# Kernel tuning notes

Measured on AMD Instinct MI355X. Metric: run time of the kernel, lower is better.

## Reference

```python
import jax, jax.numpy as jnp
import numpy as np

WIN = (4, 16)
HEADS = 4
DIM = 128
HID = 512

def _rel_index(win):
    ch = np.arange(win[0]); cw = np.arange(win[1])
    coords = np.stack(np.meshgrid(ch, cw, indexing='ij')).reshape(2, -1)  # 2, N
    rel = (coords[:, :, None] - coords[:, None, :]).transpose(1, 2, 0).astype(np.int64)  # N,N,2
    rel[:, :, 0] += win[0] - 1
    rel[:, :, 1] += win[1] - 1
    rel[:, :, 0] *= 2 * win[1] - 1
    return jnp.asarray(rel.sum(-1))  # (N, N) int

REL_IDX = _rel_index(WIN)

def _ln(x, g, b):
    m = x.mean(-1, keepdims=True)
    v = ((x - m) ** 2).mean(-1, keepdims=True)
    return (x - m) / jnp.sqrt(v + 1e-5) * g + b

def _gelu(x):
    return jax.nn.gelu(x, approximate=False)

def _posconv3d(x, w, b):
    # depthwise 3x3x3 conv with singleton depth axis; x: B,C,H,W; w: C,1,3,3,3
    y = jax.lax.conv_general_dilated(x[:, :, None], w, (1, 1, 1), ((1, 1), (1, 1), (1, 1)),
                                     feature_group_count=x.shape[1],
                                     dimension_numbers=('NCDHW', 'OIDHW', 'NCDHW'))
    return y[:, :, 0] + b[None, :, None, None]

def _dwconv2d(x, w, b):
    # depthwise 3x3 conv; x: B,Ch,H,W; w: Ch,1,3,3
    y = jax.lax.conv_general_dilated(x, w, (1, 1), ((1, 1), (1, 1)),
                                     feature_group_count=x.shape[1],
                                     dimension_numbers=('NCHW', 'OIHW', 'NCHW'))
    return y + b[None, :, None, None]

def setup_inputs() -> dict:
    key = jax.random.key(0)
    ks = jax.random.split(key, 12)
    B, C, H, W = 4, DIM, 192, 192
    s = 0.02
    return {
        'x': jax.random.normal(ks[0], (B, C, H, W), jnp.float32),
        'pos_w': jax.random.normal(ks[1], (C, 1, 3, 3, 3), jnp.float32) * s,
        'pos_b': jnp.zeros((C,), jnp.float32),
        'ln1_g': jnp.ones((C,), jnp.float32),
        'ln1_b': jnp.zeros((C,), jnp.float32),
        'q_w': jax.random.normal(ks[2], (C, C), jnp.float32) * s,
        'q_b': jnp.zeros((C,), jnp.float32),
        'kv_w': jax.random.normal(ks[3], (C, 2 * C), jnp.float32) * s,
        'kv_b': jnp.zeros((2 * C,), jnp.float32),
        'rpb': jax.random.normal(ks[4], ((2 * WIN[0] - 1) * (2 * WIN[1] - 1), HEADS), jnp.float32) * s,
        'proj_w': jax.random.normal(ks[5], (C, C), jnp.float32) * s,
        'proj_b': jnp.zeros((C,), jnp.float32),
        'fft1_w': jax.random.normal(ks[6], (2 * C, 2 * C), jnp.float32) * s,
        'fft1_b': jnp.zeros((2 * C,), jnp.float32),
        'fft2_w': jax.random.normal(ks[7], (2 * C, 2 * C), jnp.float32) * s,
        'fft2_b': jnp.zeros((2 * C,), jnp.float32),
        'ln2_g': jnp.ones((C,), jnp.float32),
        'ln2_b': jnp.zeros((C,), jnp.float32),
        'l1_w': jax.random.normal(ks[8], (C, HID), jnp.float32) * s,
        'l1_b': jnp.zeros((HID,), jnp.float32),
        'dw_w': jax.random.normal(ks[9], (HID, 1, 3, 3), jnp.float32) * s,
        'dw_b': jnp.zeros((HID,), jnp.float32),
        'l2_w': jax.random.normal(ks[10], (HID, C), jnp.float32) * s,
        'l2_b': jnp.zeros((C,), jnp.float32),
    }

def _forward(x, pos_w, pos_b, ln1_g, ln1_b, q_w, q_b, kv_w, kv_b, rpb, proj_w, proj_b,
             fft1_w, fft1_b, fft2_w, fft2_b, ln2_g, ln2_b, l1_w, l1_b, dw_w, dw_b, l2_w, l2_b):
    B, C, H, W = x.shape
    wh, ww = WIN
    N = wh * ww
    hd = C // HEADS
    # depthwise 3D positional embedding
    x = x + _posconv3d(x, pos_w, pos_b)
    xt = x.transpose(0, 2, 3, 1)  # B,H,W,C
    shortcut = xt
    xn = _ln(xt, ln1_g, ln1_b)
    # window partition: (B*nW, N, C)  (idx=0 -> no shift, no mask)
    win = xn.reshape(B, H // wh, wh, W // ww, ww, C).transpose(0, 1, 3, 2, 4, 5).reshape(-1, N, C)
    q = (win @ q_w + q_b).reshape(-1, N, HEADS, hd).transpose(0, 2, 1, 3)  # Bw,h,N,d
    kv = (win @ kv_w + kv_b).reshape(-1, N, 2, HEADS, hd).transpose(2, 0, 3, 1, 4)
    k, v = kv[0], kv[1]
    attn = jnp.einsum('bhnd,bhmd->bhnm', q * (hd ** -0.5), k)
    rel_bias = rpb[REL_IDX].transpose(2, 0, 1)  # heads,N,N
    attn = jax.nn.softmax(attn + rel_bias[None], axis=-1)
    out = jnp.einsum('bhnm,bhmd->bhnd', attn, v).transpose(0, 2, 1, 3).reshape(-1, N, C)
    out = out @ proj_w + proj_b
    out = out.reshape(B, H // wh, W // ww, wh, ww, C).transpose(0, 1, 3, 2, 4, 5).reshape(B, H, W, C)
    xt = shortcut + out
    # FFT residual branch (two 1x1 convs on cat(real,imag))
    xc = xt.transpose(0, 3, 1, 2)  # B,C,H,W
    f = jnp.fft.rfft2(xc, axes=(-2, -1))
    ff = jnp.concatenate([f.real, f.imag], axis=1)  # B,2C,H,Wf
    ff = jnp.einsum('bchw,co->bohw', ff, fft1_w) + fft1_b[None, :, None, None]
    ff = jnp.where(ff >= 0, ff, 0.01 * ff)  # LeakyReLU(0.01)
    ff = jnp.einsum('bchw,co->bohw', ff, fft2_w) + fft2_b[None, :, None, None]
    fr, fi = jnp.split(ff, 2, axis=1)
    y = jnp.fft.irfft2(fr + 1j * fi, s=(H, W), axes=(-2, -1))
    xt = xt + y.transpose(0, 2, 3, 1)
    # LeFF: linear -> dwconv -> linear, on full (H,W) grid
    xn2 = _ln(xt, ln2_g, ln2_b)
    h1 = _gelu(xn2 @ l1_w + l1_b)               # B,H,W,HID
    h1 = _gelu(_dwconv2d(h1.transpose(0, 3, 1, 2), dw_w, dw_b))
    h2 = h1.transpose(0, 2, 3, 1) @ l2_w + l2_b  # B,H,W,C
    xt = xt + h2
    return xt.transpose(0, 3, 1, 2)

def reference(x, pos_w, pos_b, ln1_g, ln1_b, q_w, q_b, kv_w, kv_b, rpb, proj_w, proj_b,
              fft1_w, fft1_b, fft2_w, fft2_b, ln2_g, ln2_b, l1_w, l1_b, dw_w, dw_b, l2_w, l2_b):
    return _forward(x, pos_w, pos_b, ln1_g, ln1_b, q_w, q_b, kv_w, kv_b, rpb, proj_w, proj_b,
                    fft1_w, fft1_b, fft2_w, fft2_b, ln2_g, ln2_b, l1_w, l1_b, dw_w, dw_b, l2_w, l2_b)
```

## Files before the change

kernel.cpp:

```cpp
#include <hip/hip_runtime.h>
#include <hip/hip_bf16.h>
#include <math.h>

#define C_DIM 128
#define HGT 192
#define WID 192
#define NB 4
#define WFD 97

#define T_BIAS  0
#define T_QKVB  16384
#define TF_SZ   16896
#define UT_MW    0
#define UT_MHF   49152
#define UT_MHI   196608
#define UT_MWI   344064
#define UT_QKVW  387072
#define UT_PROJW 436224
#define UT_FFT1W 452608
#define UT_FFT2W 518144
#define UT_L1W   583680
#define UT_L2W   649216
#define UT_TOT   714752
#define TAB_SZ   374272

typedef __attribute__((ext_vector_type(8))) short bf16x8;
typedef __attribute__((ext_vector_type(4))) float f32x4;

__device__ __forceinline__ float gelu_f(float v){
  return 0.5f*v*(1.0f + erff(v*0.70710678118654752440f));
}
__device__ __forceinline__ unsigned short f2bf(float f){
  __hip_bfloat16 h = __float2bfloat16(f);
  return *reinterpret_cast<unsigned short*>(&h);
}
__device__ __forceinline__ float bf2f(unsigned short u){
  unsigned int x = ((unsigned int)u)<<16;
  return __uint_as_float(x);
}
__device__ __forceinline__ void st8u(unsigned short* d, bf16x8 v){
  unsigned int* wp = (unsigned int*)&v;
  unsigned int* dp = (unsigned int*)d;
  dp[0]=wp[0]; dp[1]=wp[1]; dp[2]=wp[2]; dp[3]=wp[3];
}

__global__ __launch_bounds__(256) void build_tables(float* __restrict__ tab,
        const float* __restrict__ rpb, const float* __restrict__ q_b, const float* __restrict__ kv_b,
        const float* __restrict__ q_w, const float* __restrict__ kv_w, const float* __restrict__ proj_w,
        const float* __restrict__ fft1_w, const float* __restrict__ fft2_w,
        const float* __restrict__ l1_w, const float* __restrict__ l2_w){
  int idx = blockIdx.x*256 + threadIdx.x;
  const float STEP = (float)(6.283185307179586476925286766559/192.0);
  if (idx < 16384){
    int head = idx>>12, n = (idx>>6)&63, m = idx&63;
    int dh = n/16 - m/16 + 3;
    int dw = (n&15) - (m&15) + 15;
    tab[T_BIAS+idx] = rpb[(dh*31+dw)*4 + head];
    return;
  }
  idx -= 16384;
  if (idx < 384){
    tab[T_QKVB+idx] = (idx < 128) ? q_b[idx] : kv_b[idx-128];
    return;
  }
  idx -= 384;
  unsigned short* ut = (unsigned short*)(tab + TF_SZ);
  if (idx < 49152){
    int r = idx/192, w = idx%192;
    float v = 0.f;
    if (r < 97){ int a = (r*w)%192; v = cosf(a*STEP); }
    else if (r < 194){ int a = ((r-97)*w)%192; v = -sinf(a*STEP); }
    ut[UT_MW+idx] = f2bf(v);
    return;
  }
  idx -= 49152;
  if (idx < 147456){
    int r = idx/384, j = idx%384;
    int hf = (r < 192) ? r : r-192;
    int h  = (j < 192) ? j : j-192;
    int a = (hf*h)%192;
    float c = cosf(a*STEP), s = sinf(a*STEP);
    float v;
    if (r < 192) v = (j < 192) ? c : s;
    else         v = (j < 192) ? -s : c;
    ut[UT_MHF+idx] = f2bf(v);
    return;
  }
  idx -= 147456;
  if (idx < 147456){
    int r = idx/384, j = idx%384;
    int h  = (r < 192) ? r : r-192;
    int hf = (j < 192) ? j : j-192;
    int a = (h*hf)%192;
    float c = cosf(a*STEP), s = sinf(a*STEP);
    float v;
    if (r < 192) v = (j < 192) ? c : -s;
    else         v = (j < 192) ? s : c;
    ut[UT_MHI+idx] = f2bf(v);
    return;
  }
  idx -= 147456;
  if (idx < 43008){
    int w = idx/224, j = idx%224;
    float v = 0.f;
    if (j < 97){
      int a = (j*w)%192;
      float sc = ((j==0 || j==96) ? 1.f : 2.f) / 36864.f;
      v = sc*cosf(a*STEP);
    } else if (j >= 112 && j < 209){
      int k = j-112;
      int a = (k*w)%192;
      float sc = ((k==0 || k==96) ? 1.f : 2.f) / 36864.f;
      v = -sc*sinf(a*STEP);
    }
    ut[UT_MWI+idx] = f2bf(v);
    return;
  }
  idx -= 43008;
  if (idx < 49152){
    int n = idx/128, k = idx%128;
    float v = (n < 128) ? q_w[(size_t)k*128 + n] : kv_w[(size_t)k*256 + (n-128)];
    ut[UT_QKVW+idx] = f2bf(v);
    return;
  }
  idx -= 49152;
  if (idx < 16384){
    int n = idx/128, k = idx%128;
    ut[UT_PROJW+idx] = f2bf(proj_w[(size_t)k*128 + n]);
    return;
  }
  idx -= 16384;
  if (idx < 65536){
    int n = idx/256, k = idx%256;
    ut[UT_FFT1W+idx] = f2bf(fft1_w[(size_t)k*256 + n]);
    return;
  }
  idx -= 65536;
  if (idx < 65536){
    int n = idx/256, k = idx%256;
    ut[UT_FFT2W+idx] = f2bf(fft2_w[(size_t)k*256 + n]);
    return;
  }
  idx -= 65536;
  if (idx < 65536){
    int n = idx/128, k = idx%128;
    ut[UT_L1W+idx] = f2bf(l1_w[(size_t)k*512 + n]);
    return;
  }
  idx -= 65536;
  if (idx < 65536){
    int n = idx/512, k = idx%512;
    ut[UT_L2W+idx] = f2bf(l2_w[(size_t)k*128 + n]);
  }
}

__global__ __launch_bounds__(256) void posconv3_kernel(const float* __restrict__ x, const float* __restrict__ pw,
                               const float* __restrict__ pb, float* __restrict__ xt){
  __shared__ float rows_s[16*340];
  int w0 = blockIdx.x*32, h0 = blockIdx.y*8;
  int b = blockIdx.z >> 3, cb = (blockIdx.z & 7)*16;
  int tid = threadIdx.x;
  int hl = tid >> 5, wl = tid & 31;
  for (int e = tid; e < 16*340; e += 256){
    int c = e / 340; int rem = e - c*340;
    int r = rem / 34; int wc = rem - r*34;
    int gh = h0 - 1 + r, gw = w0 - 1 + wc;
    float v = 0.f;
    if (gh >= 0 && gh < HGT && gw >= 0 && gw < WID)
      v = x[((size_t)(b*C_DIM + cb + c))*(HGT*WID) + gh*WID + gw];
    rows_s[e] = v;
  }
  __syncthreads();
  float outr[16];
  #pragma unroll
  for (int c = 0; c < 16; ++c){
    const float* rs = &rows_s[c*340];
    float wreg[9];
    #pragma unroll
    for (int t9 = 0; t9 < 9; ++t9) wreg[t9] = pw[(cb+c)*27 + 9 + t9];
    float bias = pb[cb+c];
    float acc = rs[(hl+1)*34 + wl+1] + bias;
    #pragma unroll
    for (int ky = 0; ky < 3; ++ky)
      #pragma unroll
      for (int kx = 0; kx < 3; ++kx)
        acc += wreg[ky*3+kx]*rs[(hl+ky)*34 + wl+kx];
    outr[c] = acc;
  }
  __syncthreads();
  {
    int px = hl*32 + wl;
    #pragma unroll
    for (int c = 0; c < 16; ++c) rows_s[px*17 + c] = outr[c];
  }
  __syncthreads();
  for (int r = 0; r < 16; ++r){
    int e = r*256 + tid;
    int cl = e & 15, hw = e >> 4;
    int h = hw >> 5, w = hw & 31;
    xt[((size_t)(b*HGT + h0+h)*WID + (w0+w))*C_DIM + cb + cl] = rows_s[hw*17 + cl];
  }
}

__global__ __launch_bounds__(256) void ln_stats_kernel(const float* __restrict__ src, float* __restrict__ stats){
  int wave = threadIdx.x >> 6; int lane = threadIdx.x & 63;
  size_t p = (size_t)blockIdx.x*4 + wave;
  const float* s = src + p*C_DIM;
  float v0 = s[lane], v1 = s[lane+64];
  float sum = v0 + v1;
  #pragma unroll
  for (int o=1; o<64; o<<=1) sum += __shfl_xor(sum, o, 64);
  float m = sum * (1.0f/128.0f);
  float d0 = v0-m, d1 = v1-m;
  float vs = d0*d0 + d1*d1;
  #pragma unroll
  for (int o=1; o<64; o<<=1) vs += __shfl_xor(vs, o, 64);
  float rstd = rsqrtf(vs*(1.0f/128.0f) + 1e-5f);
  if (lane==0){ stats[2*p] = m; stats[2*p+1] = rstd; }
}

template<int ACT, bool ADD, bool LNA, bool ABF, bool OBF, int NT>
__global__ __launch_bounds__(256) void gemm2(const void* __restrict__ A1v,
                            const unsigned short* __restrict__ WT, const float* __restrict__ bias,
                            void* __restrict__ dstv, int K, int N, int lda,
                            const float* __restrict__ stats, const float* __restrict__ lng,
                            const float* __restrict__ lnb, int prow0, int pmax){
  __shared__ __align__(16) unsigned short As[64*40];
  __shared__ __align__(16) unsigned short Bs[NT][64*40];
  int p0 = blockIdx.y*64, n00 = blockIdx.x*(64*NT);
  int tid = threadIdx.x;
  int wave = tid >> 6, lane = tid & 63;
  int wr = (wave>>1)*32, wc = (wave&1)*32;
  f32x4 acc[NT][4];
  #pragma unroll
  for (int nt=0; nt<NT; ++nt)
    #pragma unroll
    for (int q=0; q<4; ++q) acc[nt][q] = (f32x4){};
  int am = tid >> 2, ak = (tid & 3)*8;
  int brow = tid >> 2, bkk = (tid & 3)*8;
  for (int k0 = 0; k0 < K; k0 += 32){
    if constexpr (ABF){
      const unsigned short* A1u = (const unsigned short*)A1v;
      bf16x8 av = *(const bf16x8*)(A1u + (size_t)(p0+am)*lda + k0 + ak);
      st8u(&As[am*40 + ak], av);
    } else {
      int gp = p0 + am;
      float s0 = 0.f, s1 = 0.f;
      if (LNA){
        gp += prow0;
        gp = gp < 0 ? 0 : (gp > pmax ? pmax : gp);
        s0 = stats[2*gp]; s1 = stats[2*gp+1];
      }
      const float* src = (const float*)A1v + (size_t)gp*lda + k0 + ak;
      float4 aa = *(const float4*)src;
      float4 ab = *(const float4*)(src+4);
      float v[8] = {aa.x,aa.y,aa.z,aa.w,ab.x,ab.y,ab.z,ab.w};
      unsigned short* dp = &As[am*40 + ak];
      #pragma unroll
      for (int j=0;j<8;j++){
        float f = v[j];
        if (LNA) f = (f - s0)*s1*lng[k0+ak+j] + lnb[k0+ak+j];
        dp[j] = f2bf(f);
      }
    }
    #pragma unroll
    for (int nt=0; nt<NT; ++nt){
      bf16x8 wv = *(const bf16x8*)(WT + (size_t)(n00 + nt*64 + brow)*K + k0 + bkk);
      st8u(&Bs[nt][brow*40 + bkk], wv);
    }
    __syncthreads();
    int fm = lane & 15, kg = (lane>>4)*8;
    bf16x8 a0 = *(const bf16x8*)&As[(wr+fm)*40 + kg];
    bf16x8 a1 = *(const bf16x8*)&As[(wr+16+fm)*40 + kg];
    #pragma unroll
    for (int nt=0; nt<NT; ++nt){
      bf16x8 b0 = *(const bf16x8*)&Bs[nt][(wc+fm)*40 + kg];
      bf16x8 b1 = *(const bf16x8*)&Bs[nt][(wc+16+fm)*40 + kg];
      acc[nt][0] = __builtin_amdgcn_mfma_f32_16x16x32_bf16(a0, b0, acc[nt][0], 0,0,0);
      acc[nt][1] = __builtin_amdgcn_mfma_f32_16x16x32_bf16(a0, b1, acc[nt][1], 0,0,0);
      acc[nt][2] = __builtin_amdgcn_mfma_f32_16x16x32_bf16(a1, b0, acc[nt][2], 0,0,0);
      acc[nt][3] = __builtin_amdgcn_mfma_f32_16x16x32_bf16(a1, b1, acc[nt][3], 0,0,0);
    }
    __syncthreads();
  }
  int cn = lane & 15, rq = (lane>>4)*4;
  #pragma unroll
  for (int nt=0; nt<NT; ++nt){
    #pragma unroll
    for (int mi=0; mi<2; ++mi){
      #pragma unroll
      for (int ni=0; ni<2; ++ni){
        f32x4 a = acc[nt][mi*2+ni];
        int n = n00 + nt*64 + wc + ni*16 + cn;
        float bsv = bias[n];
        #pragma unroll
        for (int r=0; r<4; ++r){
          size_t row = (size_t)p0 + wr + mi*16 + rq + r;
          float v = a[r] + bsv;
          if (ACT==1) v = (v>=0.f) ? v : 0.01f*v;
          if (ACT==2) v = gelu_f(v);
          if constexpr (OBF){
            ((unsigned short*)dstv)[row*(size_t)N + n] = f2bf(v);
          } else {
            float* dst = (float*)dstv;
            if (ADD) v += dst[row*(size_t)N + n];
            dst[row*(size_t)N + n] = v;
          }
        }
      }
    }
  }
}

template<int MODE>
__global__ __launch_bounds__(256) void dft_gemm(const unsigned short* __restrict__ Atab,
                            const void* __restrict__ W1v, const void* __restrict__ W2v,
                            void* __restrict__ D1v, void* __restrict__ D2v, int k0){
  constexpr int K      = (MODE==0)?192 : (MODE==3)?224 : 384;
  constexpr int MT     = (MODE==0)?4 : (MODE==3)?3 : 6;
  constexpr int MVALID = (MODE==0)?194 : (MODE==3)?192 : 384;
  __shared__ __align__(16) unsigned short As[64*40];
  __shared__ __align__(16) unsigned short Bs[64*40];
  int slab = blockIdx.y / MT;
  int p0 = (blockIdx.y % MT)*64, n0 = blockIdx.x*64;
  int tid = threadIdx.x;
  int wave = tid >> 6, lane = tid & 63;
  int wr = (wave>>1)*32, wc = (wave&1)*32;
  f32x4 acc00 = {}, acc01 = {}, acc10 = {}, acc11 = {};
  int am = tid >> 2, ak = (tid & 3)*8;
  int bk = tid >> 3, bn = (tid & 7)*8;
  for (int kk0 = 0; kk0 < K; kk0 += 32){
    {
      bf16x8 av = *(const bf16x8*)(Atab + (size_t)(p0+am)*K + kk0 + ak);
      st8u(&As[am*40 + ak], av);
    }
    {
      int r = kk0 + bk;
      if (MODE==0){
        const float* src = (const float*)W1v + (size_t)slab*24576 + (size_t)r*128 + n0 + bn;
        float4 wa = *(const float4*)src;
        float4 wb = *(const float4*)(src+4);
        float v[8] = {wa.x,wa.y,wa.z,wa.w,wb.x,wb.y,wb.z,wb.w};
        #pragma unroll
        for (int j=0;j<8;j++) Bs[(bn+j)*40 + bk] = f2bf(v[j]);
      } else {
        const unsigned short* src;
        if (MODE==1) src = (r<192) ? (const unsigned short*)W1v + (size_t)(k0+slab)*128 + (size_t)r*12416
                                   : (const unsigned short*)W2v + (size_t)(k0+slab)*128 + (size_t)(r-192)*12416;
        else if (MODE==2) src = (r<192) ? (const unsigned short*)W1v + (size_t)slab*49152 + (size_t)r*256
                                        : (const unsigned short*)W2v + (size_t)slab*49152 + (size_t)(r-192)*256;
        else src = (r<112) ? (const unsigned short*)W1v + (size_t)slab*24832 + (size_t)r*256
                           : (const unsigned short*)W2v + (size_t)slab*24832 + (size_t)(r-112)*256;
        src += n0 + bn;
        bf16x8 wv = *(const bf16x8*)src;
        #pragma unroll
        for (int j=0;j<8;j++) Bs[(bn+j)*40 + bk] = (unsigned short)wv[j];
      }
    }
    __syncthreads();
    int fm = lane & 15, kg = (lane>>4)*8;
    bf16x8 a0 = *(const bf16x8*)&As[(wr+fm)*40 + kg];
    bf16x8 a1 = *(const bf16x8*)&As[(wr+16+fm)*40 + kg];
    bf16x8 b0 = *(const bf16x8*)&Bs[(wc+fm)*40 + kg];
    bf16x8 b1 = *(const bf16x8*)&Bs[(wc+16+fm)*40 + kg];
    acc00 = __builtin_amdgcn_mfma_f32_16x16x32_bf16(a0, b0, acc00, 0,0,0);
    acc01 = __builtin_amdgcn_mfma_f32_16x16x32_bf16(a0, b1, acc01, 0,0,0);
    acc10 = __builtin_amdgcn_mfma_f32_16x16x32_bf16(a1, b0, acc10, 0,0,0);
    acc11 = __builtin_amdgcn_mfma_f32_16x16x32_bf16(a1, b1, acc11, 0,0,0);
    __syncthreads();
  }
  int cn = lane & 15, rq = (lane>>4)*4;
  #pragma unroll
  for (int mi=0; mi<2; ++mi){
    #pragma unroll
    for (int ni=0; ni<2; ++ni){
      f32x4 a = (mi==0) ? (ni==0?acc00:acc01) : (ni==0?acc10:acc11);
      int n = n0 + wc + ni*16 + cn;
      #pragma unroll
      for (int r=0; r<4; ++r){
        int p = p0 + wr + mi*16 + rq + r;
        if (p >= MVALID) continue;
        float v = a[r];
        if (MODE==0){
          unsigned short* D1 = (unsigned short*)D1v;
          unsigned short* D2 = (unsigned short*)D2v;
          if (p < 97) D1[(size_t)slab*12416 + (size_t)p*128 + n] = f2bf(v);
          else        D2[(size_t)slab*12416 + (size_t)(p-97)*128 + n] = f2bf(v);
        } else if (MODE==1){
          unsigned short* base = (unsigned short*)D1v + (size_t)slab*49152;
          if (p < 192) base[(size_t)p*256 + n] = f2bf(v);
          else         base[(size_t)(p-192)*256 + 128 + n] = f2bf(v);
        } else if (MODE==2){
          unsigned short* D1 = (unsigned short*)D1v;
          int kg2 = k0 + slab;
          if (p < 192) D1[((size_t)p*97 + kg2)*256 + n] = f2bf(v);
          else         D1[((size_t)(p-192)*97 + kg2)*256 + 128 + n] = f2bf(v);
        } else {
          ((float*)D1v)[(size_t)slab*24576 + (size_t)p*128 + n] += v;
        }
      }
    }
  }
}

#define XS_OFF  0
#define WQK_OFF 8704
#define VT_OFF  29184
#define SHM_TOT 38400
__global__ __launch_bounds__(256) void attn_fused3(
    float* __restrict__ XT, const float* __restrict__ stats,
    const float* __restrict__ g1, const float* __restrict__ b1,
    const unsigned short* __restrict__ QKVW, const float* __restrict__ QKVB,
    const float* __restrict__ biasT, const unsigned short* __restrict__ PROJW,
    const float* __restrict__ projb){
  __shared__ __align__(16) unsigned short shm[SHM_TOT];
  int win = blockIdx.x;
  int b = win/576, rem = win%576, whi = rem/12, wwi = rem%12;
  int tid = threadIdx.x, wave = tid>>6, lane = tid&63, head = wave;
  int fm = lane & 15, kg = (lane>>4)*8;
  size_t rowbase = (size_t)(b*HGT + whi*4)*WID + wwi*16;
  {
    int t = tid >> 2;
    int c0 = (tid & 3)*32;
    size_t grow = rowbase + (size_t)(t>>4)*WID + (t&15);
    const float* src = XT + grow*C_DIM + c0;
    float m = stats[2*grow], rs = stats[2*grow+1];
    unsigned short* dst = &shm[XS_OFF + t*136 + c0];
    #pragma unroll
    for (int j=0;j<32;j++){
      float f = (src[j]-m)*rs*g1[c0+j] + b1[c0+j];
      dst[j] = f2bf(f);
    }
  }
  __syncthreads();
  unsigned short* Qw = &shm[WQK_OFF + wave*5120];
  unsigned short* Kw = Qw + 2560;
  unsigned short* Vt = &shm[VT_OFF + wave*2304];
  #pragma unroll
  for (int op=0; op<3; ++op){
    f32x4 acc[4][2];
    #pragma unroll
    for (int tf=0; tf<4; ++tf){ acc[tf][0] = (f32x4){}; acc[tf][1] = (f32x4){}; }
    int wrow0 = op*128 + head*32;
    #pragma unroll
    for (int kk0=0; kk0<128; kk0+=32){
      bf16x8 bfr0 = *(const bf16x8*)(QKVW + (size_t)(wrow0 + fm)*128 + kk0 + kg);
      bf16x8 bfr1 = *(const bf16x8*)(QKVW + (size_t)(wrow0 + 16 + fm)*128 + kk0 + kg);
      #pragma unroll
      for (int tf=0; tf<4; ++tf){
        bf16x8 af = *(const bf16x8*)&shm[XS_OFF + (tf*16+fm)*136 + kk0 + kg];
        acc[tf][0] = __builtin_amdgcn_mfma_f32_16x16x32_bf16(af, bfr0, acc[tf][0], 0,0,0);
        acc[tf][1] = __builtin_amdgcn_mfma_f32_16x16x32_bf16(af, bfr1, acc[tf][1], 0,0,0);
      }
    }
    #pragma unroll
    for (int tf=0; tf<4; ++tf){
      #pragma unroll
      for (int cf=0; cf<2; ++cf){
        int n = cf*16 + fm;
        float bsv = QKVB[op*128 + head*32 + n];
        #pragma unroll
        for (int r=0;r<4;r++){
          int token = tf*16 + (lane>>4)*4 + r;
          float v = acc[tf][cf][r] + bsv;
          if (op==0) v *= 0.17677669529663688f;
          unsigned short bv = f2bf(v);
          if (op==0)      Qw[token*40 + n] = bv;
          else if (op==1) Kw[token*40 + n] = bv;
          else            Vt[n*72 + token] = bv;
        }
      }
    }
  }
  __syncthreads();
  bf16x8 qf[4], kf[4];
  #pragma unroll
  for (int t4=0; t4<4; ++t4){
    qf[t4] = *(const bf16x8*)&Qw[(t4*16+fm)*40 + kg];
    kf[t4] = *(const bf16x8*)&Kw[(t4*16+fm)*40 + kg];
  }
  f32x4 s[4][4];
  #pragma unroll
  for (int ni=0; ni<4; ++ni)
    #pragma unroll
    for (int mj=0; mj<4; ++mj){
      f32x4 z = {};
      s[ni][mj] = __builtin_amdgcn_mfma_f32_16x16x32_bf16(qf[ni], kf[mj], z, 0,0,0);
    }
  const float* bp = biasT + head*4096;
  #pragma unroll
  for (int ni=0; ni<4; ++ni){
    int nbase = ni*16 + (lane>>4)*4;
    #pragma unroll
    for (int mj=0; mj<4; ++mj){
      int m = mj*16 + fm;
      #pragma unroll
      for (int r=0;r<4;r++)
        s[ni][mj][r] += bp[(nbase+r)*64 + m];
    }
  }
  float rs_[4][4];
  #pragma unroll
  for (int ni=0; ni<4; ++ni){
    #pragma unroll
    for (int r=0;r<4;r++){
      float t = fmaxf(fmaxf(s[ni][0][r], s[ni][1][r]), fmaxf(s[ni][2][r], s[ni][3][r]));
      #pragma unroll
      for (int o=1;o<16;o<<=1) t = fmaxf(t, __shfl_xor(t, o, 64));
      float sum = 0.f;
      #pragma unroll
      for (int mj=0; mj<4; ++mj){
        float e = __expf(s[ni][mj][r] - t);
        s[ni][mj][r] = e;
        sum += e;
      }
      #pragma unroll
      for (int o=1;o<16;o<<=1) sum += __shfl_xor(sum, o, 64);
      rs_[ni][r] = sum;
    }
  }
  __syncthreads();
  unsigned short* Ps = Qw;
  #pragma unroll
  for (int ni=0; ni<4; ++ni){
    int nbase = ni*16 + (lane>>4)*4;
    #pragma unroll
    for (int mj=0; mj<4; ++mj){
      int m = mj*16 + fm;
      #pragma unroll
      for (int r=0;r<4;r++)
        Ps[(nbase+r)*72 + m] = f2bf(s[ni][mj][r]);
    }
  }
  f32x4 o2[4][2];
  #pragma unroll
  for (int ni=0; ni<4; ++ni){ o2[ni][0] = (f32x4){}; o2[ni][1] = (f32x4){}; }
  #pragma unroll
  for (int ks=0; ks<2; ++ks){
    bf16x8 vb0 = *(const bf16x8*)&Vt[fm*72 + ks*32+kg];
    bf16x8 vb1 = *(const bf16x8*)&Vt[(16+fm)*72 + ks*32+kg];
    #pragma unroll
    for (int ni=0; ni<4; ++ni){
      bf16x8 pa = *(const bf16x8*)&Ps[(ni*16+fm)*72 + ks*32+kg];
      o2[ni][0] = __builtin_amdgcn_mfma_f32_16x16x32_bf16(pa, vb0, o2[ni][0], 0,0,0);
      o2[ni][1] = __builtin_amdgcn_mfma_f32_16x16x32_bf16(pa, vb1, o2[ni][1], 0,0,0);
    }
  }
  #pragma unroll
  for (int ni=0; ni<4; ++ni){
    #pragma unroll
    for (int r=0;r<4;r++){
      int token = ni*16 + (lane>>4)*4 + r;
      float inv = 1.0f / rs_[ni][r];
      unsigned short* op = &shm[XS_OFF + token*136 + head*32];
      op[fm]    = f2bf(o2[ni][0][r]*inv);
      op[16+fm] = f2bf(o2[ni][1][r]*inv);
    }
  }
  __syncthreads();
  {
    f32x4 pacc[4][2];
    #pragma unroll
    for (int tf=0; tf<4; ++tf){ pacc[tf][0] = (f32x4){}; pacc[tf][1] = (f32x4){}; }
    int wrow0 = wave*32;
    #pragma unroll
    for (int kk0=0; kk0<128; kk0+=32){
      bf16x8 bfr0 = *(const bf16x8*)(PROJW + (size_t)(wrow0 + fm)*128 + kk0 + kg);
      bf16x8 bfr1 = *(const bf16x8*)(PROJW + (size_t)(wrow0 + 16 + fm)*128 + kk0 + kg);
      #pragma unroll
      for (int tf=0; tf<4; ++tf){
        bf16x8 af = *(const bf16x8*)&shm[XS_OFF + (tf*16+fm)*136 + kk0 + kg];
        pacc[tf][0] = __builtin_amdgcn_mfma_f32_16x16x32_bf16(af, bfr0, pacc[tf][0], 0,0,0);
        pacc[tf][1] = __builtin_amdgcn_mfma_f32_16x16x32_bf16(af, bfr1, pacc[tf][1], 0,0,0);
      }
    }
    #pragma unroll
    for (int tf=0; tf<4; ++tf){
      #pragma unroll
      for (int cf=0; cf<2; ++cf){
        int n = wave*32 + cf*16 + fm;
        float bsv = projb[n];
        #pragma unroll
        for (int r=0;r<4;r++){
          size_t l = rowbase + (size_t)tf*WID + (lane>>4)*4 + r;
          XT[l*C_DIM + n] += pacc[tf][cf][r] + bsv;
        }
      }
    }
  }
}

__global__ __launch_bounds__(256) void dwconv_strip(const unsigned short* __restrict__ SB1,
                                                    const float* __restrict__ dw,
                                                    const float* __restrict__ db,
                                                    unsigned short* __restrict__ SB2,
                                                    int r0){
  int blk = blockIdx.x;
  int wt = blk % 12, hl = blk / 12;
  int tid = threadIdx.x;
  int c4 = tid & 127, ph = tid >> 7;
  int ch = c4*4;
  int w0 = wt*16 + ph*8;
  int h = r0 + hl;
  float wreg[9][4], bias[4];
  #pragma unroll
  for (int j=0;j<4;j++){
    bias[j] = db[ch+j];
    #pragma unroll
    for (int t9=0;t9<9;t9++) wreg[t9][j] = dw[(ch+j)*9+t9];
  }
  const unsigned short* rp[3];
  bool rv[3];
  #pragma unroll
  for (int ky=0;ky<3;ky++){
    int hh = h + ky - 1;
    rv[ky] = (hh >= 0) && (hh < HGT);
    rp[ky] = SB1 + ((size_t)(hl+ky)*WID)*512 + ch;
  }
  float win[3][3][4];
  #pragma unroll
  for (int ky=0;ky<3;ky++){
    #pragma unroll
    for (int j=0;j<4;j++){ win[ky][0][j]=0.f; win[ky][1][j]=0.f; }
    if (rv[ky]){
      if (w0 > 0){
        const unsigned int* p = (const unsigned int*)(rp[ky] + (size_t)(w0-1)*512);
        unsigned int u0=p[0], u1=p[1];
        win[ky][0][0]=bf2f((unsigned short)(u0&0xFFFF)); win[ky][0][1]=bf2f((unsigned short)(u0>>16));
        win[ky][0][2]=bf2f((unsigned short)(u1&0xFFFF)); win[ky][0][3]=bf2f((unsigned short)(u1>>16));
      }
      {
        const unsigned int* p = (const unsigned int*)(rp[ky] + (size_t)w0*512);
        unsigned int u0=p[0], u1=p[1];
        win[ky][1][0]=bf2f((unsigned short)(u0&0xFFFF)); win[ky][1][1]=bf2f((unsigned short)(u0>>16));
        win[ky][1][2]=bf2f((unsigned short)(u1&0xFFFF)); win[ky][1][3]=bf2f((unsigned short)(u1>>16));
      }
    }
  }
  #pragma unroll
  for (int px=0; px<8; ++px){
    int w = w0 + px;
    #pragma unroll
    for (int ky=0;ky<3;ky++){
      #pragma unroll
      for (int j=0;j<4;j++) win[ky][2][j]=0.f;
      if (rv[ky] && (w+1) < WID){
        const unsigned int* p = (const unsigned int*)(rp[ky] + (size_t)(w+1)*512);
        unsigned int u0=p[0], u1=p[1];
        win[ky][2][0]=bf2f((unsigned short)(u0&0xFFFF)); win[ky][2][1]=bf2f((unsigned short)(u0>>16));
        win[ky][2][2]=bf2f((unsigned short)(u1&0xFFFF)); win[ky][2][3]=bf2f((unsigned short)(u1>>16));
      }
    }
    float a[4];
    #pragma unroll
    for (int j=0;j<4;j++){
      float acc = bias[j];
      #pragma unroll
      for (int ky=0;ky<3;ky++)
        #pragma unroll
        for (int kx=0;kx<3;kx++)
          acc += wreg[ky*3+kx][j]*win[ky][kx][j];
      a[j] = gelu_f(acc);
    }
    unsigned int o0 = (unsigned int)f2bf(a[0]) | ((unsigned int)f2bf(a[1])<<16);
    unsigned int o1 = (unsigned int)f2bf(a[2]) | ((unsigned int)f2bf(a[3])<<16);
    unsigned int* op = (unsigned int*)&SB2[((size_t)hl*WID + w)*512 + ch];
    op[0] = o0; op[1] = o1;
    #pragma unroll
    for (int ky=0;ky<3;ky++)
      #pragma unroll
      for (int j=0;j<4;j++){ win[ky][0][j]=win[ky][1][j]; win[ky][1][j]=win[ky][2][j]; }
  }
}

__global__ __launch_bounds__(256) void transpose_b_kernel(const float* __restrict__ src, float* __restrict__ dst,
                                                          size_t zstride){
  __shared__ float tile[128*65];
  int w0 = blockIdx.x*64, h = blockIdx.y;
  size_t zo = (size_t)blockIdx.z * zstride;
  int tid = threadIdx.x;
  for (int r=0; r<32; r++){
    int e = tid + 256*r; int c = e & 127, wl = e >> 7;
    tile[c*65 + wl] = src[zo + ((size_t)h*WID + w0 + wl)*C_DIM + c];
  }
  __syncthreads();
  for (int r=0; r<32; r++){
    int e = tid + 256*r; int wl = e & 63, c = e >> 6;
    dst[zo + ((size_t)c*HGT + h)*WID + w0 + wl] = tile[c*65 + wl];
  }
}

extern "C" void kernel_launch(void* const* d_in, const int* in_sizes, int n_in,
                              void* d_out, int out_size, void* d_ws, size_t ws_size,
                              hipStream_t stream) {
  const float* x      = (const float*)d_in[0];
  const float* pos_w  = (const float*)d_in[1];
  const float* pos_b  = (const float*)d_in[2];
  const float* ln1_g  = (const float*)d_in[3];
  const float* ln1_b  = (const float*)d_in[4];
  const float* q_w    = (const float*)d_in[5];
  const float* q_b    = (const float*)d_in[6];
  const float* kv_w   = (const float*)d_in[7];
  const float* kv_b   = (const float*)d_in[8];
  const float* rpb    = (const float*)d_in[9];
  const float* proj_w = (const float*)d_in[10];
  const float* proj_b = (const float*)d_in[11];
  const float* fft1_w = (const float*)d_in[12];
  const float* fft1_b = (const float*)d_in[13];
  const float* fft2_w = (const float*)d_in[14];
  const float* fft2_b = (const float*)d_in[15];
  const float* ln2_g  = (const float*)d_in[16];
  const float* ln2_b  = (const float*)d_in[17];
  const float* l1_w   = (const float*)d_in[18];
  const float* l1_b   = (const float*)d_in[19];
  const float* dw_w   = (const float*)d_in[20];
  const float* dw_b   = (const float*)d_in[21];
  const float* l2_w   = (const float*)d_in[22];
  const float* l2_b   = (const float*)d_in[23];

  const size_t S   = (size_t)NB*HGT*WID*C_DIM;
  const size_t Sb  = S/NB;
  const size_t SZb = (size_t)HGT*WFD*C_DIM;
  const size_t GSZ = (size_t)HGT*WFD*256;
  const int    P   = (int)(NB*HGT*WID);

  float* ws    = (float*)d_ws;
  float* TAB   = ws;
  float* STATS = ws + TAB_SZ;
  float* POOL  = ws + TAB_SZ + 2*(size_t)P;
  size_t head  = TAB_SZ + 2*(size_t)P;
  size_t pool  = (ws_size/4 > head) ? (ws_size/4 - head) : 0;

  bool xt_in_pool = (pool >= S + 11000000);
  float* XT     = xt_in_pool ? POOL : (float*)d_out;
  float* POOL2  = xt_in_pool ? POOL + S : POOL;
  size_t pool2  = xt_in_pool ? pool - S : pool;

  const float* biasT = TAB + T_BIAS;
  const float* QKVB  = TAB + T_QKVB;
  const unsigned short* UT = (const unsigned short*)(TAB + TF_SZ);
  const unsigned short* MW  = UT + UT_MW;
  const unsigned short* MHF = UT + UT_MHF;
  const unsigned short* MHI = UT + UT_MHI;
  const unsigned short* MWI = UT + UT_MWI;
  const unsigned short* QKVW  = UT + UT_QKVW;
  const unsigned short* PROJW = UT + UT_PROJW;
  const unsigned short* FFT1W = UT + UT_FFT1W;
  const unsigned short* FFT2W = UT + UT_FFT2W;
  const unsigned short* L1W   = UT + UT_L1W;
  const unsigned short* L2W   = UT + UT_L2W;

  build_tables<<<2858, 256, 0, stream>>>(TAB, rpb, q_b, kv_b, q_w, kv_w, proj_w,
                                         fft1_w, fft2_w, l1_w, l2_w);
  posconv3_kernel<<<dim3(6,24,32), 256, 0, stream>>>(x, pos_w, pos_b, XT);

  ln_stats_kernel<<<P/4, 256, 0, stream>>>(XT, STATS);
  attn_fused3<<<2304, 256, 0, stream>>>(XT, STATS, ln1_g, ln1_b, QKVW, QKVB,
                                        biasT, PROJW, proj_b);

  {
    unsigned short* FRu = (unsigned short*)POOL2;
    unsigned short* FIu = FRu + SZb;
    unsigned short* Gu  = FIu + SZb;
    size_t fixed = SZb + GSZ/2;
    int CKmax = 1;
    if (pool2 > fixed + 49152) CKmax = (int)((pool2 - fixed)/49152);
    if (CKmax < 1) CKmax = 1;
    if (CKmax > WFD) CKmax = WFD;
    int nch = (WFD + CKmax - 1)/CKmax;
    int CK = (WFD + nch - 1)/nch;
    unsigned short* FF0u = (unsigned short*)(POOL2 + fixed);
    unsigned short* FF1u = FF0u + (size_t)CK*49152;
    for (int b = 0; b < NB; ++b){
      float* XTb = XT + (size_t)b*Sb;
      dft_gemm<0><<<dim3(2, 192*4), 256, 0, stream>>>(MW, XTb, nullptr, FRu, FIu, 0);
      for (int k0 = 0; k0 < WFD; k0 += CK){
        int ck = (WFD - k0 < CK) ? (WFD - k0) : CK;
        int rows = ck*192;
        dft_gemm<1><<<dim3(2, ck*6), 256, 0, stream>>>(MHF, FRu, FIu, FF0u, nullptr, k0);
        gemm2<1,false,false,true,true,1><<<dim3(4, rows/64), 256, 0, stream>>>(
            FF0u, FFT1W, fft1_b, FF1u, 256, 256, 256, nullptr, nullptr, nullptr, 0, 0);
        gemm2<0,false,false,true,true,1><<<dim3(4, rows/64), 256, 0, stream>>>(
            FF1u, FFT2W, fft2_b, FF0u, 256, 256, 256, nullptr, nullptr, nullptr, 0, 0);
        dft_gemm<2><<<dim3(2, ck*6), 256, 0, stream>>>(MHI, FF0u, FF0u+128, Gu, nullptr, k0);
      }
      dft_gemm<3><<<dim3(2, 192*3), 256, 0, stream>>>(MWI, Gu, Gu+128, XTb, nullptr, 0);
    }
  }

  ln_stats_kernel<<<P/4, 256, 0, stream>>>(XT, STATS);

  {
    int SH = 96;
    while ((size_t)(3*SH+4)*49152 > pool2 && SH > 24) SH >>= 1;
    const size_t SB1SZ = (size_t)(SH+2)*98304;
    unsigned short* SB1u[2] = { (unsigned short*)POOL2, (unsigned short*)POOL2 + SB1SZ };
    unsigned short* SB2u = (unsigned short*)POOL2 + 2*SB1SZ;
    int nStrips = HGT/SH;
    for (int b = 0; b < NB; ++b){
      auto launch_g = [&](int s){
        int r0 = s*SH;
        int prow0 = (b*HGT + r0 - 1)*WID;
        gemm2<2,false,true,false,true,2><<<dim3(4, (SH+2)*3), 256, 0, stream>>>(
            XT, L1W, l1_b, SB1u[s&1], 128, 512, 128,
            STATS, ln2_g, ln2_b, prow0, P-1);
      };
      launch_g(0);
      for (int s = 0; s < nStrips; ++s){
        if (s+1 < nStrips) launch_g(s+1);
        int r0 = s*SH;
        dwconv_strip<<<12*SH, 256, 0, stream>>>(SB1u[s&1], dw_w, dw_b, SB2u, r0);
        gemm2<0,true,false,true,false,1><<<dim3(2, SH*3), 256, 0, stream>>>(
            SB2u, L2W, l2_b, XT + ((size_t)(b*HGT + r0)*WID)*C_DIM,
            512, 128, 512, nullptr, nullptr, nullptr, 0, 0);
      }
    }
  }

  if (xt_in_pool){
    transpose_b_kernel<<<dim3(3,192,4), 256, 0, stream>>>(XT, (float*)d_out, Sb);
  } else {
    for (int b = 0; b < NB; ++b){
      transpose_b_kernel<<<dim3(3,192,1), 256, 0, stream>>>(XT + (size_t)b*Sb, POOL2, 0);
      hipMemcpyAsync((float*)d_out + (size_t)b*Sb, POOL2, Sb*sizeof(float),
                     hipMemcpyDeviceToDevice, stream);
    }
  }
}
```

Before: 1.153 ms.

## Fuse output transpose into final GEMM and use output buffer for FFT chunks

The last LeFF GEMM gains a transposed-output mode: it adds the residual from XT, stages the tile in shared memory, and writes NCHW directly to the output, so the separate transpose pass is no longer needed. The threshold for keeping XT in the workspace is lowered. When XT is in the workspace, the still-unused output buffer holds the FFT intermediate buffers so all 97 frequency columns are processed in one chunk, which cuts launch count. This depends on the output buffer being large enough for both FF buffers and on its contents being fully overwritten afterwards.

Result: faster. 1.112 ms, median of 2 (-3.6%).

```diff
diff --git a/kernel.cpp b/kernel.cpp
--- a/kernel.cpp
+++ b/kernel.cpp
@@ -219,7 +219,7 @@
   if (lane==0){ stats[2*p] = m; stats[2*p+1] = rstd; }
 }
 
-template<int ACT, bool ADD, bool LNA, bool ABF, bool OBF, int NT>
+template<int ACT, bool ADD, bool LNA, bool ABF, bool OBF, int NT, bool OUTT = false>
 __global__ __launch_bounds__(256) void gemm2(const void* __restrict__ A1v,
                             const unsigned short* __restrict__ WT, const float* __restrict__ bias,
                             void* __restrict__ dstv, int K, int N, int lda,
@@ -227,6 +227,7 @@
                             const float* __restrict__ lnb, int prow0, int pmax){
   __shared__ __align__(16) unsigned short As[64*40];
   __shared__ __align__(16) unsigned short Bs[NT][64*40];
+  __shared__ float tileT[OUTT ? 64*66 : 1];
   int p0 = blockIdx.y*64, n00 = blockIdx.x*(64*NT);
   int tid = threadIdx.x;
   int wave = tid >> 6, lane = tid & 63;
@@ -284,27 +285,59 @@
     __syncthreads();
   }
   int cn = lane & 15, rq = (lane>>4)*4;
-  #pragma unroll
-  for (int nt=0; nt<NT; ++nt){
+  if constexpr (OUTT){
+    const float* XTres = stats;
+    int p0b = prow0 + p0;
     #pragma unroll
     for (int mi=0; mi<2; ++mi){
       #pragma unroll
       for (int ni=0; ni<2; ++ni){
-        f32x4 a = acc[nt][mi*2+ni];
-        int n = n00 + nt*64 + wc + ni*16 + cn;
-        float bsv = bias[n];
+        f32x4 a = acc[0][mi*2+ni];
+        int nl = wc + ni*16 + cn;
+        float bsv = bias[n00 + nl];
         #pragma unroll
         for (int r=0; r<4; ++r){
-          size_t row = (size_t)p0 + wr + mi*16 + rq + r;
+          int rowl = wr + mi*16 + rq + r;
           float v = a[r] + bsv;
-          if (ACT==1) v = (v>=0.f) ? v : 0.01f*v;
-          if (ACT==2) v = gelu_f(v);
-          if constexpr (OBF){
-            ((unsigned short*)dstv)[row*(size_t)N + n] = f2bf(v);
-          } else {
-            float* dst = (float*)dstv;
-            if (ADD) v += dst[row*(size_t)N + n];
-            dst[row*(size_t)N + n] = v;
+          v += XTres[(size_t)(p0b + rowl)*C_DIM + n00 + nl];
+          tileT[rowl*66 + nl] = v;
+        }
+      }
+    }
+    __syncthreads();
+    int bb = p0b/36864;
+    int hh = (p0b/192)%192;
+    int w0 = p0b%192;
+    float* dout = (float*)dstv;
+    #pragma unroll
+    for (int it=0; it<16; ++it){
+      int e = it*256 + tid;
+      int c = e >> 6, wl = e & 63;
+      dout[((size_t)bb*C_DIM + n00 + c)*36864 + (size_t)hh*192 + w0 + wl] = tileT[wl*66 + c];
+    }
+  } else {
+    #pragma unroll
+    for (int nt=0; nt<NT; ++nt){
+      #pragma unroll
+      for (int mi=0; mi<2; ++mi){
+        #pragma unroll
+        for (int ni=0; ni<2; ++ni){
+          f32x4 a = acc[nt][mi*2+ni];
+          int n = n00 + nt*64 + wc + ni*16 + cn;
+          float bsv = bias[n];
+          #pragma unroll
+          for (int r=0; r<4; ++r){
+            size_t row = (size_t)p0 + wr + mi*16 + rq + r;
+            float v = a[r] + bsv;
+            if (ACT==1) v = (v>=0.f) ? v : 0.01f*v;
+            if (ACT==2) v = gelu_f(v);
+            if constexpr (OBF){
+              ((unsigned short*)dstv)[row*(size_t)N + n] = f2bf(v);
+            } else {
+              float* dst = (float*)dstv;
+              if (ADD) v += dst[row*(size_t)N + n];
+              dst[row*(size_t)N + n] = v;
+            }
           }
         }
       }
@@ -731,7 +764,7 @@
   size_t head  = TAB_SZ + 2*(size_t)P;
   size_t pool  = (ws_size/4 > head) ? (ws_size/4 - head) : 0;
 
-  bool xt_in_pool = (pool >= S + 11000000);
+  bool xt_in_pool = (pool >= S + 5200000);
   float* XT     = xt_in_pool ? POOL : (float*)d_out;
   float* POOL2  = xt_in_pool ? POOL + S : POOL;
   size_t pool2  = xt_in_pool ? pool - S : pool;
@@ -763,14 +796,23 @@
     unsigned short* FIu = FRu + SZb;
     unsigned short* Gu  = FIu + SZb;
     size_t fixed = SZb + GSZ/2;
-    int CKmax = 1;
-    if (pool2 > fixed + 49152) CKmax = (int)((pool2 - fixed)/49152);
-    if (CKmax < 1) CKmax = 1;
-    if (CKmax > WFD) CKmax = WFD;
-    int nch = (WFD + CKmax - 1)/CKmax;
-    int CK = (WFD + nch - 1)/nch;
-    unsigned short* FF0u = (unsigned short*)(POOL2 + fixed);
-    unsigned short* FF1u = FF0u + (size_t)CK*49152;
+    int CK;
+    unsigned short* FF0u;
+    unsigned short* FF1u;
+    if (xt_in_pool){
+      CK = WFD;
+      FF0u = (unsigned short*)d_out;
+      FF1u = FF0u + (size_t)WFD*49152;
+    } else {
+      int CKmax = 1;
+      if (pool2 > fixed + 49152) CKmax = (int)((pool2 - fixed)/49152);
+      if (CKmax < 1) CKmax = 1;
+      if (CKmax > WFD) CKmax = WFD;
+      int nch = (WFD + CKmax - 1)/CKmax;
+      CK = (WFD + nch - 1)/nch;
+      FF0u = (unsigned short*)(POOL2 + fixed);
+      FF1u = FF0u + (size_t)CK*49152;
+    }
     for (int b = 0; b < NB; ++b){
       float* XTb = XT + (size_t)b*Sb;
       dft_gemm<0><<<dim3(2, 192*4), 256, 0, stream>>>(MW, XTb, nullptr, FRu, FIu, 0);
@@ -810,16 +852,20 @@
         if (s+1 < nStrips) launch_g(s+1);
         int r0 = s*SH;
         dwconv_strip<<<12*SH, 256, 0, stream>>>(SB1u[s&1], dw_w, dw_b, SB2u, r0);
-        gemm2<0,true,false,true,false,1><<<dim3(2, SH*3), 256, 0, stream>>>(
-            SB2u, L2W, l2_b, XT + ((size_t)(b*HGT + r0)*WID)*C_DIM,
-            512, 128, 512, nullptr, nullptr, nullptr, 0, 0);
-      }
-    }
-  }
-
-  if (xt_in_pool){
-    transpose_b_kernel<<<dim3(3,192,4), 256, 0, stream>>>(XT, (float*)d_out, Sb);
-  } else {
+        if (xt_in_pool){
+          gemm2<0,false,false,true,false,1,true><<<dim3(2, SH*3), 256, 0, stream>>>(
+              SB2u, L2W, l2_b, d_out, 512, 128, 512,
+              XT, nullptr, nullptr, (b*HGT + r0)*WID, 0);
+        } else {
+          gemm2<0,true,false,true,false,1><<<dim3(2, SH*3), 256, 0, stream>>>(
+              SB2u, L2W, l2_b, XT + ((size_t)(b*HGT + r0)*WID)*C_DIM,
+              512, 128, 512, nullptr, nullptr, nullptr, 0, 0);
+        }
+      }
+    }
+  }
+
+  if (!xt_in_pool){
     for (int b = 0; b < NB; ++b){
       transpose_b_kernel<<<dim3(3,192,1), 256, 0, stream>>>(XT + (size_t)b*Sb, POOL2, 0);
       hipMemcpyAsync((float*)d_out + (size_t)b*Sb, POOL2, Sb*sizeof(float),
```
